# Performance work log

Hardware: AMD Instinct MI355X
Metric: run time of the kernel (lower is better)

Reference implementation:

```python
import jax, jax.numpy as jnp
import numpy as np

BITS = 4
GROUP = 128
IN_F = 4096
OUT_F = 4096
MASK = (1 << BITS) - 1  # 15
# non-uniform 4-bit codebook from QuantLinear (AF / AbnormalFloat style)
CODE = jnp.array([-6, -4, -3, -2, -1.5, -1, -0.5, -0.0,
                   0.0, 0.5, 1, 1.5, 2, 3, 4, 6], dtype=jnp.float32)


def setup_inputs() -> dict:
    key = jax.random.key(0)
    k1, k2, k3, k4, k5 = jax.random.split(key, 5)
    x = jax.random.normal(k1, (4, 2048, IN_F), dtype=jnp.float32)
    qweight = jax.random.randint(k2, (IN_F // 32 * BITS, OUT_F), 0, 2147483647, dtype=jnp.int32)
    n_groups = IN_F // GROUP
    scales = jax.random.uniform(k3, (n_groups, OUT_F), dtype=jnp.float32, minval=0.01, maxval=0.1)
    scales2 = jax.random.uniform(k4, (n_groups, OUT_F), dtype=jnp.float32, minval=0.01, maxval=0.1)
    bias = jax.random.normal(k5, (OUT_F,), dtype=jnp.float32)
    return {"x": x, "qweight": qweight, "scales": scales, "scales2": scales2, "bias": bias}


def dequantize(qweight, scales, scales2):
    # unpack: (rows, OUT) -> (rows, 8, OUT) nibbles; matches torch right_shift + & maxq
    wf = jnp.arange(0, 32, BITS, dtype=jnp.int32)          # (8,)
    q = (qweight[:, None, :] >> wf[None, :, None]) & MASK  # (IN/8, 8, OUT) ints in [0,15]
    q = q.reshape(IN_F // GROUP, GROUP, OUT_F)             # group-major layout
    w = CODE[q]                                            # codebook lookup
    # two-scale: positive codes use scales, negative codes use scales2 (per group, per out-col)
    w = jnp.where(w >= 0, w * scales[:, None, :], w * scales2[:, None, :])
    return w.reshape(IN_F, OUT_F)


def reference(x, qweight, scales, scales2, bias):
    W = dequantize(qweight, scales, scales2)        # (IN_F, OUT_F)
    out = jnp.einsum('bsi,io->bso', x, W) + bias    # grouped-dequant matmul + bias
    return out
```

## Files before the change

### kernel.cpp

```cpp
#include <hip/hip_runtime.h>
#include <hip/hip_bf16.h>
#include <stdint.h>

#define M_ROWS 8192
#define K_DIM  4096
#define N_DIM  4096

using bf16 = __hip_bfloat16;
typedef __attribute__((ext_vector_type(4))) float f32x4;
typedef __attribute__((ext_vector_type(8))) short s16x8;

__device__ __forceinline__ void gll16(const bf16* g, bf16* l) {
  __builtin_amdgcn_global_load_lds(
      (const __attribute__((address_space(1))) void*)g,
      (__attribute__((address_space(3))) void*)l, 16, 0, 0);
}

__global__ __launch_bounds__(256) void prep_k(
    const int* __restrict__ qw, const float* __restrict__ s1,
    const float* __restrict__ s2, const float* __restrict__ x,
    bf16* __restrict__ Bp, bf16* __restrict__ Ap)
{
  const int bid = blockIdx.x;
  if (bid < 2048) {
    const int t = bid * 256 + threadIdx.x;
    const int o = t & 4095;
    const int q = t >> 12;
    const int r0 = q << 2;
    const int g = r0 >> 4;
    const int nt = o >> 8, col = o & 255;
    const int sw = (col >> 1) & 3;
    const float a = s1[g * 4096 + o] * 0.5f;
    const float b = s2[g * 4096 + o] * 0.5f;
    const uint64_t lo = 0x00FFFEFDFCFAF8F4ull;
    const uint64_t hi = 0x0C08060403020100ull;
    bf16* dst = Bp + (((size_t)(nt * 128 + q)) << 13) + col * 32;
    #pragma unroll
    for (int j = 0; j < 4; ++j) {
      const uint32_t wbits = (uint32_t)qw[(size_t)(r0 + j) * 4096 + o];
      union { bf16 h[8]; s16x8 v; } u;
      #pragma unroll
      for (int i = 0; i < 8; ++i) {
        const int qc = (wbits >> (4 * i)) & 15;
        const uint64_t pk = (qc & 8) ? hi : lo;
        const int c2 = (int)(int8_t)(uint8_t)(pk >> ((qc & 7) * 8));
        const float sc = (qc & 8) ? a : b;
        u.h[i] = __float2bfloat16((float)c2 * sc);
      }
      *(s16x8*)(dst + ((j ^ sw) << 3)) = u.v;
    }
  } else {
    const int t = (bid - 2048) * 256 + threadIdx.x;
    const int k8 = t & 511;
    const int kt = k8 >> 2;
    const int s_lin = k8 & 3;
    const int m  = t >> 9;
    const int tm = m >> 7, row = m & 127;
    const float* s = x + (size_t)m * 4096 + k8 * 8;
    f32x4 v0 = *(const f32x4*)s;
    f32x4 v1 = *(const f32x4*)(s + 4);
    union { bf16 h[8]; s16x8 v; } u;
    #pragma unroll
    for (int j = 0; j < 4; ++j) {
      u.h[j]     = __float2bfloat16(v0[j]);
      u.h[4 + j] = __float2bfloat16(v1[j]);
    }
    const int ss = s_lin ^ ((row >> 1) & 3);
    bf16* dst = Ap + (((size_t)(tm * 128 + kt)) << 12) + row * 32 + ss * 8;
    *(s16x8*)dst = u.v;
  }
}

#define BAR()                                                         \
    asm volatile("s_barrier" ::: "memory");                           \
    __builtin_amdgcn_sched_barrier(0)

#define VMW(N)                                                        \
    asm volatile("s_waitcnt vmcnt(" #N ")" ::: "memory");             \
    __builtin_amdgcn_sched_barrier(0)

#define KT9(BUF, KTN, PRE, VM)                                        \
  {                                                                   \
    const bf16* L_ = &lds[BUF][0];                                    \
    _Pragma("unroll")                                                 \
    for (int m = 0; m < 4; ++m) af[m] = *(const s16x8*)(L_ + aoff + m * 512); \
    _Pragma("unroll")                                                 \
    for (int n = 0; n < 4; ++n) bb[n] = *(const s16x8*)(L_ + boff + n * 512); \
    if (PRE) stage((KTN), ((BUF) + 2) % 3);                           \
    __builtin_amdgcn_s_setprio(1);                                    \
    _Pragma("unroll")                                                 \
    for (int m = 0; m < 4; ++m) {                                     \
      _Pragma("unroll")                                               \
      for (int n = 0; n < 4; ++n)                                     \
        acc[m][n] = __builtin_amdgcn_mfma_f32_16x16x32_bf16(          \
            af[m], bb[n], acc[m][n], 0, 0, 0);                        \
    }                                                                 \
    __builtin_amdgcn_s_setprio(0);                                    \
    VMW(VM);                                                          \
    BAR();                                                            \
  }

__global__ __launch_bounds__(512, 4) void gemm9_k(
    const bf16* __restrict__ Ap, const bf16* __restrict__ Bp,
    const float* __restrict__ bias, float* __restrict__ out)
{
  __shared__ bf16 lds[3][12288];

  const int id  = blockIdx.x;
  const int xcd = id & 7, lid = id >> 3;
  const int tn  = lid >> 3;
  const int tm  = xcd * 8 + (lid & 7);
  const int tid = (int)threadIdx.x;
  const int lane = tid & 63;
  const int w   = tid >> 6;
  const int wr  = w >> 2;
  const int wc  = w & 3;
  const int lr  = lane & 15;
  const int lg  = lane >> 4;
  const int sl  = (lg ^ ((lr >> 1) & 3)) << 3;
  const int aoff = (wr * 64 + lr) * 32 + sl;
  const int boff = 4096 + (wc * 64 + lr) * 32 + sl;

  const bf16* Abase = Ap + ((size_t)tm << 19);
  const bf16* Bbase = Bp + ((size_t)tn << 20);

  f32x4 acc[4][4];
  #pragma unroll
  for (int m = 0; m < 4; ++m)
    #pragma unroll
    for (int n = 0; n < 4; ++n) acc[m][n] = (f32x4){0.f, 0.f, 0.f, 0.f};

  auto stage = [&](int kt, int buf) {
    gll16(Abase + ((size_t)kt << 12) + tid * 8, &lds[buf][tid * 8]);
    const bf16* bs = Bbase + ((size_t)kt << 13) + tid * 8;
    gll16(bs,        &lds[buf][4096 + tid * 8]);
    gll16(bs + 4096, &lds[buf][8192 + tid * 8]);
  };

  s16x8 af[4], bb[4];

  stage(0, 0);
  stage(1, 1);
  VMW(3);
  BAR();

  #pragma unroll 1
  for (int t3 = 0; t3 < 42; ++t3) {
    KT9(0, 3 * t3 + 2, 1, 3);
    KT9(1, 3 * t3 + 3, 1, 3);
    KT9(2, 3 * t3 + 4, 1, 3);
  }
  KT9(0, 0, 0, 0);
  KT9(1, 0, 0, 0);

  const int orow0 = tm * 128 + wr * 64 + lg * 4;
  const int ocol0 = tn * 256 + wc * 64 + lr;
  float bv[4];
  #pragma unroll
  for (int n = 0; n < 4; ++n) bv[n] = bias[ocol0 + n * 16];
  #pragma unroll
  for (int m = 0; m < 4; ++m) {
    #pragma unroll
    for (int r = 0; r < 4; ++r) {
      float* op = out + (size_t)(orow0 + m * 16 + r) * N_DIM + ocol0;
      #pragma unroll
      for (int n = 0; n < 4; ++n) op[n * 16] = acc[m][n][r] + bv[n];
    }
  }
}

__global__ __launch_bounds__(256) void dequant_f(
    const int* __restrict__ qw, const float* __restrict__ s1,
    const float* __restrict__ s2, bf16* __restrict__ Bp)
{
  const int t = blockIdx.x * 256 + threadIdx.x;
  const int o = t & 4095;
  const int r = t >> 12;
  const int g = r >> 4;
  const int kt = r >> 2;
  const int kk0 = (r & 3) * 8;
  const uint32_t wbits = (uint32_t)qw[(size_t)r * 4096 + o];
  const float a = s1[g * 4096 + o] * 0.5f;
  const float b = s2[g * 4096 + o] * 0.5f;
  const uint64_t lo = 0x00FFFEFDFCFAF8F4ull;
  const uint64_t hi = 0x0C08060403020100ull;
  union { bf16 h[8]; s16x8 v; } u;
  #pragma unroll
  for (int j = 0; j < 8; ++j) {
    const int q = (wbits >> (4 * j)) & 15;
    const uint64_t pk = (q & 8) ? hi : lo;
    const int c2 = (int)(int8_t)(uint8_t)(pk >> ((q & 7) * 8));
    const float s = (q & 8) ? a : b;
    u.h[j] = __float2bfloat16((float)c2 * s);
  }
  const int nt = o >> 7, col = o & 127;
  bf16* dst = Bp + (((size_t)(nt * 128 + kt) * 128 + col) * 32 + kk0);
  *(s16x8*)dst = u.v;
}

__global__ __launch_bounds__(256) void gemmf_k(
    const float* __restrict__ x, const bf16* __restrict__ Bp,
    const float* __restrict__ bias, float* __restrict__ out)
{
  __shared__ bf16 As[2][4096];
  __shared__ bf16 Bs[2][4096];

  const int id  = blockIdx.x;
  const int swz = (id & 7) * 256 + (id >> 3);
  const int tm  = swz >> 5;
  const int tn  = swz & 31;
  const int tid = threadIdx.x;
  const int lane = tid & 63;
  const int w   = tid >> 6;
  const int wr  = (w >> 1) * 64;
  const int wc  = (w & 1) * 64;
  const int lr  = lane & 15;
  const int lg  = lane >> 4;

  f32x4 acc[4][4];
  #pragma unroll
  for (int m = 0; m < 4; ++m)
    #pragma unroll
    for (int n = 0; n < 4; ++n) acc[m][n] = (f32x4){0.f, 0.f, 0.f, 0.f};

  const bf16* bsrc = Bp + ((size_t)tn << 19);
  const float* asrc_f = x + ((size_t)(tm * 128 + (tid >> 1)) << 12) + (tid & 1) * 16;
  float areg[16];

  auto stageB = [&](int kt, int buf) {
    const bf16* bs = bsrc + ((size_t)kt << 12);
    gll16(bs + tid * 8,        &Bs[buf][tid * 8]);
    gll16(bs + 2048 + tid * 8, &Bs[buf][2048 + tid * 8]);
  };
  auto loadA = [&](int kt) {
    const float* s = asrc_f + ((size_t)kt << 5);
    #pragma unroll
    for (int i = 0; i < 4; ++i)
      *(f32x4*)(areg + i * 4) = *(const f32x4*)(s + i * 4);
  };
  auto writeA = [&](int buf) {
    union { bf16 h[16]; s16x8 v[2]; } u;
    #pragma unroll
    for (int i = 0; i < 16; ++i) u.h[i] = __float2bfloat16(areg[i]);
    bf16* d = &As[buf][(tid >> 1) * 32 + (tid & 1) * 16];
    *(s16x8*)d = u.v[0];
    *(s16x8*)(d + 8) = u.v[1];
  };
  auto compute = [&](int buf) {
    s16x8 af[4], bv[4];
    #pragma unroll
    for (int m = 0; m < 4; ++m)
      af[m] = *(const s16x8*)(&As[buf][(wr + m * 16 + lr) * 32 + lg * 8]);
    #pragma unroll
    for (int n = 0; n < 4; ++n)
      bv[n] = *(const s16x8*)(&Bs[buf][(wc + n * 16 + lr) * 32 + lg * 8]);
    #pragma unroll
    for (int m = 0; m < 4; ++m)
      #pragma unroll
      for (int n = 0; n < 4; ++n)
        acc[m][n] = __builtin_amdgcn_mfma_f32_16x16x32_bf16(af[m], bv[n],
                                                            acc[m][n], 0, 0, 0);
  };

  stageB(0, 0);
  loadA(0);
  writeA(0);
  __syncthreads();

  #pragma unroll 2
  for (int kt = 0; kt < 128; ++kt) {
    const int buf = kt & 1;
    if (kt + 1 < 128) {
      stageB(kt + 1, buf ^ 1);
      loadA(kt + 1);
    }
    compute(buf);
    if (kt + 1 < 128) writeA(buf ^ 1);
    __syncthreads();
  }

  const int orow0 = tm * 128 + wr + lg * 4;
  const int ocol0 = tn * 128 + wc + lr;
  float bvv[4];
  #pragma unroll
  for (int n = 0; n < 4; ++n) bvv[n] = bias[ocol0 + n * 16];
  #pragma unroll
  for (int m = 0; m < 4; ++m) {
    #pragma unroll
    for (int r = 0; r < 4; ++r) {
      float* op = out + (size_t)(orow0 + m * 16 + r) * N_DIM + ocol0;
      #pragma unroll
      for (int n = 0; n < 4; ++n)
        op[n * 16] = acc[m][n][r] + bvv[n];
    }
  }
}

extern "C" void kernel_launch(void* const* d_in, const int* in_sizes, int n_in,
                              void* d_out, int out_size, void* d_ws, size_t ws_size,
                              hipStream_t stream) {
  const float* x    = (const float*)d_in[0];
  const int*   qw   = (const int*)d_in[1];
  const float* s1   = (const float*)d_in[2];
  const float* s2   = (const float*)d_in[3];
  const float* bias = (const float*)d_in[4];
  float* out = (float*)d_out;

  const size_t BP_BYTES = (size_t)K_DIM * N_DIM * 2;
  const size_t XB_BYTES = (size_t)M_ROWS * K_DIM * 2;
  bf16* Bp = (bf16*)d_ws;

  if (ws_size >= BP_BYTES + XB_BYTES) {
    bf16* Ap = (bf16*)((char*)d_ws + BP_BYTES);
    prep_k<<<dim3(18432), dim3(256), 0, stream>>>(qw, s1, s2, x, Bp, Ap);
    gemm9_k<<<dim3(1024), dim3(512), 0, stream>>>(Ap, Bp, bias, out);
  } else {
    dequant_f<<<dim3(8192), dim3(256), 0, stream>>>(qw, s1, s2, Bp);
    gemmf_k<<<dim3(2048), dim3(256), 0, stream>>>(x, Bp, bias, out);
  }
}
```

Measured before the change: 267.5 us.

## Fuse fp32-to-bf16 conversion of activations into GEMM main loop

Result: no change. 272.1 us (+1.7%).

```diff
diff --git a/kernel.cpp b/kernel.cpp
--- a/kernel.cpp
+++ b/kernel.cpp
@@ -18,56 +18,33 @@
 
 __global__ __launch_bounds__(256) void prep_k(
     const int* __restrict__ qw, const float* __restrict__ s1,
-    const float* __restrict__ s2, const float* __restrict__ x,
-    bf16* __restrict__ Bp, bf16* __restrict__ Ap)
+    const float* __restrict__ s2, bf16* __restrict__ Bp)
 {
-  const int bid = blockIdx.x;
-  if (bid < 2048) {
-    const int t = bid * 256 + threadIdx.x;
-    const int o = t & 4095;
-    const int q = t >> 12;
-    const int r0 = q << 2;
-    const int g = r0 >> 4;
-    const int nt = o >> 8, col = o & 255;
-    const int sw = (col >> 1) & 3;
-    const float a = s1[g * 4096 + o] * 0.5f;
-    const float b = s2[g * 4096 + o] * 0.5f;
-    const uint64_t lo = 0x00FFFEFDFCFAF8F4ull;
-    const uint64_t hi = 0x0C08060403020100ull;
-    bf16* dst = Bp + (((size_t)(nt * 128 + q)) << 13) + col * 32;
-    #pragma unroll
-    for (int j = 0; j < 4; ++j) {
-      const uint32_t wbits = (uint32_t)qw[(size_t)(r0 + j) * 4096 + o];
-      union { bf16 h[8]; s16x8 v; } u;
-      #pragma unroll
-      for (int i = 0; i < 8; ++i) {
-        const int qc = (wbits >> (4 * i)) & 15;
-        const uint64_t pk = (qc & 8) ? hi : lo;
-        const int c2 = (int)(int8_t)(uint8_t)(pk >> ((qc & 7) * 8));
-        const float sc = (qc & 8) ? a : b;
-        u.h[i] = __float2bfloat16((float)c2 * sc);
-      }
-      *(s16x8*)(dst + ((j ^ sw) << 3)) = u.v;
-    }
-  } else {
-    const int t = (bid - 2048) * 256 + threadIdx.x;
-    const int k8 = t & 511;
-    const int kt = k8 >> 2;
-    const int s_lin = k8 & 3;
-    const int m  = t >> 9;
-    const int tm = m >> 7, row = m & 127;
-    const float* s = x + (size_t)m * 4096 + k8 * 8;
-    f32x4 v0 = *(const f32x4*)s;
-    f32x4 v1 = *(const f32x4*)(s + 4);
+  const int t = blockIdx.x * 256 + threadIdx.x;
+  const int o = t & 4095;
+  const int q = t >> 12;
+  const int r0 = q << 2;
+  const int g = r0 >> 4;
+  const int nt = o >> 8, col = o & 255;
+  const int sw = (col >> 1) & 3;
+  const float a = s1[g * 4096 + o] * 0.5f;
+  const float b = s2[g * 4096 + o] * 0.5f;
+  const uint64_t lo = 0x00FFFEFDFCFAF8F4ull;
+  const uint64_t hi = 0x0C08060403020100ull;
+  bf16* dst = Bp + (((size_t)(nt * 128 + q)) << 13) + col * 32;
+  #pragma unroll
+  for (int j = 0; j < 4; ++j) {
+    const uint32_t wbits = (uint32_t)qw[(size_t)(r0 + j) * 4096 + o];
     union { bf16 h[8]; s16x8 v; } u;
     #pragma unroll
-    for (int j = 0; j < 4; ++j) {
-      u.h[j]     = __float2bfloat16(v0[j]);
-      u.h[4 + j] = __float2bfloat16(v1[j]);
-    }
-    const int ss = s_lin ^ ((row >> 1) & 3);
-    bf16* dst = Ap + (((size_t)(tm * 128 + kt)) << 12) + row * 32 + ss * 8;
-    *(s16x8*)dst = u.v;
+    for (int i = 0; i < 8; ++i) {
+      const int qc = (wbits >> (4 * i)) & 15;
+      const uint64_t pk = (qc & 8) ? hi : lo;
+      const int c2 = (int)(int8_t)(uint8_t)(pk >> ((qc & 7) * 8));
+      const float sc = (qc & 8) ? a : b;
+      u.h[i] = __float2bfloat16((float)c2 * sc);
+    }
+    *(s16x8*)(dst + ((j ^ sw) << 3)) = u.v;
   }
 }
 
@@ -75,18 +52,28 @@
     asm volatile("s_barrier" ::: "memory");                           \
     __builtin_amdgcn_sched_barrier(0)
 
+#define LGKM0()                                                       \
+    asm volatile("s_waitcnt lgkmcnt(0)" ::: "memory");                \
+    __builtin_amdgcn_sched_barrier(0)
+
 #define VMW(N)                                                        \
     asm volatile("s_waitcnt vmcnt(" #N ")" ::: "memory");             \
     __builtin_amdgcn_sched_barrier(0)
 
-#define KT9(BUF, KTN, PRE, VM)                                        \
+#define KT(BUF, T, PRE_A, PRE_B, VM)                                  \
   {                                                                   \
     const bf16* L_ = &lds[BUF][0];                                    \
     _Pragma("unroll")                                                 \
     for (int m = 0; m < 4; ++m) af[m] = *(const s16x8*)(L_ + aoff + m * 512); \
     _Pragma("unroll")                                                 \
     for (int n = 0; n < 4; ++n) bb[n] = *(const s16x8*)(L_ + boff + n * 512); \
-    if (PRE) stage((KTN), ((BUF) + 2) % 3);                           \
+    if (PRE_A) {                                                      \
+      const float* xs = xsrc + (size_t)((T) + 1) * 32;                \
+      va0 = *(const f32x4*)xs;                                        \
+      va1 = *(const f32x4*)(xs + 4);                                  \
+    }                                                                 \
+    if (PRE_B) gllB((T) + 2, ((BUF) + 2) % 3);                        \
+    __builtin_amdgcn_sched_barrier(0);                                \
     __builtin_amdgcn_s_setprio(1);                                    \
     _Pragma("unroll")                                                 \
     for (int m = 0; m < 4; ++m) {                                     \
@@ -96,12 +83,23 @@
             af[m], bb[n], acc[m][n], 0, 0, 0);                        \
     }                                                                 \
     __builtin_amdgcn_s_setprio(0);                                    \
+    __builtin_amdgcn_sched_barrier(0);                                \
+    if (PRE_A) {                                                      \
+      union { bf16 h[8]; s16x8 v; } u;                                \
+      _Pragma("unroll")                                               \
+      for (int j = 0; j < 4; ++j) {                                   \
+        u.h[j]     = __float2bfloat16(va0[j]);                        \
+        u.h[4 + j] = __float2bfloat16(va1[j]);                        \
+      }                                                               \
+      *(s16x8*)(&lds[((BUF) + 1) % 3][awoff]) = u.v;                  \
+    }                                                                 \
+    LGKM0();                                                          \
     VMW(VM);                                                          \
     BAR();                                                            \
   }
 
 __global__ __launch_bounds__(512, 4) void gemm9_k(
-    const bf16* __restrict__ Ap, const bf16* __restrict__ Bp,
+    const float* __restrict__ x, const bf16* __restrict__ Bp,
     const float* __restrict__ bias, float* __restrict__ out)
 {
   __shared__ bf16 lds[3][12288];
@@ -121,7 +119,11 @@
   const int aoff = (wr * 64 + lr) * 32 + sl;
   const int boff = 4096 + (wc * 64 + lr) * 32 + sl;
 
-  const bf16* Abase = Ap + ((size_t)tm << 19);
+  const int arow = tid >> 2;
+  const int aslot = tid & 3;
+  const float* xsrc = x + (size_t)(tm * 128 + arow) * 4096 + aslot * 8;
+  const int awoff = arow * 32 + ((aslot ^ ((arow >> 1) & 3)) << 3);
+
   const bf16* Bbase = Bp + ((size_t)tn << 20);
 
   f32x4 acc[4][4];
@@ -130,28 +132,40 @@
     #pragma unroll
     for (int n = 0; n < 4; ++n) acc[m][n] = (f32x4){0.f, 0.f, 0.f, 0.f};
 
-  auto stage = [&](int kt, int buf) {
-    gll16(Abase + ((size_t)kt << 12) + tid * 8, &lds[buf][tid * 8]);
+  auto gllB = [&](int kt, int buf) {
     const bf16* bs = Bbase + ((size_t)kt << 13) + tid * 8;
     gll16(bs,        &lds[buf][4096 + tid * 8]);
     gll16(bs + 4096, &lds[buf][8192 + tid * 8]);
   };
 
   s16x8 af[4], bb[4];
-
-  stage(0, 0);
-  stage(1, 1);
-  VMW(3);
+  f32x4 va0, va1;
+
+  va0 = *(const f32x4*)xsrc;
+  va1 = *(const f32x4*)(xsrc + 4);
+  gllB(0, 0);
+  {
+    union { bf16 h[8]; s16x8 v; } u;
+    #pragma unroll
+    for (int j = 0; j < 4; ++j) {
+      u.h[j]     = __float2bfloat16(va0[j]);
+      u.h[4 + j] = __float2bfloat16(va1[j]);
+    }
+    *(s16x8*)(&lds[0][awoff]) = u.v;
+  }
+  gllB(1, 1);
+  LGKM0();
+  VMW(2);
   BAR();
 
   #pragma unroll 1
   for (int t3 = 0; t3 < 42; ++t3) {
-    KT9(0, 3 * t3 + 2, 1, 3);
-    KT9(1, 3 * t3 + 3, 1, 3);
-    KT9(2, 3 * t3 + 4, 1, 3);
-  }
-  KT9(0, 0, 0, 0);
-  KT9(1, 0, 0, 0);
+    KT(0, (3 * t3),     1, 1, 2);
+    KT(1, (3 * t3 + 1), 1, 1, 2);
+    KT(2, (3 * t3 + 2), 1, 1, 2);
+  }
+  KT(0, 126, 1, 0, 0);
+  KT(1, 127, 0, 0, 0);
 
   const int orow0 = tm * 128 + wr * 64 + lg * 4;
   const int ocol0 = tn * 256 + wc * 64 + lr;
@@ -307,13 +321,11 @@
   float* out = (float*)d_out;
 
   const size_t BP_BYTES = (size_t)K_DIM * N_DIM * 2;
-  const size_t XB_BYTES = (size_t)M_ROWS * K_DIM * 2;
   bf16* Bp = (bf16*)d_ws;
 
-  if (ws_size >= BP_BYTES + XB_BYTES) {
-    bf16* Ap = (bf16*)((char*)d_ws + BP_BYTES);
-    prep_k<<<dim3(18432), dim3(256), 0, stream>>>(qw, s1, s2, x, Bp, Ap);
-    gemm9_k<<<dim3(1024), dim3(512), 0, stream>>>(Ap, Bp, bias, out);
+  if (ws_size >= BP_BYTES) {
+    prep_k<<<dim3(2048), dim3(256), 0, stream>>>(qw, s1, s2, Bp);
+    gemm9_k<<<dim3(1024), dim3(512), 0, stream>>>(x, Bp, bias, out);
   } else {
     dequant_f<<<dim3(8192), dim3(256), 0, stream>>>(qw, s1, s2, Bp);
     gemmf_k<<<dim3(2048), dim3(256), 0, stream>>>(x, Bp, bias, out);
```
